# Performance work log

Hardware: AMD Instinct MI355X
Metric: run time of the kernel (lower is better)

The kernel has to match this reference:

```python
import jax, jax.numpy as jnp
import numpy as np

B, SQ, SE, H, NH = 2, 2048, 2048, 1024, 16
HD = H // NH  # 64

def setup_inputs() -> dict:
    key = jax.random.key(0)
    ks = jax.random.split(key, 8)
    s = 1.0 / np.sqrt(H)
    return {
        "hidden_states": jax.random.normal(ks[0], (B, SQ, H), jnp.float32),
        "encoder_hidden_states": jax.random.normal(ks[1], (B, SE, H), jnp.float32),
        "attention_mask": jnp.zeros((B, 1, 1, SQ + SE), jnp.float32),
        "Wq": jax.random.normal(ks[2], (H, H), jnp.float32) * s,
        "bq": jnp.zeros((H,), jnp.float32),
        "Wk": jax.random.normal(ks[3], (H, H), jnp.float32) * s,
        "bk": jnp.zeros((H,), jnp.float32),
        "Wv": jax.random.normal(ks[4], (H, H), jnp.float32) * s,
        "bv": jnp.zeros((H,), jnp.float32),
    }

def _split_heads(x):
    # [B, S, H] -> [B, NH, S, HD]
    b, s, _ = x.shape
    return x.reshape(b, s, NH, HD).transpose(0, 2, 1, 3)

def reference(hidden_states, encoder_hidden_states, attention_mask, Wq, bq, Wk, bk, Wv, bv):
    # Q from self tokens; K,V from concat(self, encoder) along sequence
    all_hs = jnp.concatenate([hidden_states, encoder_hidden_states], axis=1)  # [B, SQ+SE, H]
    q = _split_heads(hidden_states @ Wq + bq)   # [B, NH, SQ, HD]
    k = _split_heads(all_hs @ Wk + bk)          # [B, NH, SKV, HD]
    v = _split_heads(all_hs @ Wv + bv)          # [B, NH, SKV, HD]
    scores = jnp.einsum('bhqd,bhkd->bhqk', q, k) / jnp.sqrt(jnp.float32(HD))
    scores = scores + attention_mask            # additive mask, broadcast [B,1,1,SKV]
    probs = jax.nn.softmax(scores, axis=-1)     # dropout p=0 (eval)
    ctx = jnp.einsum('bhqk,bhkd->bhqd', probs, v)
    ctx = ctx.transpose(0, 2, 1, 3).reshape(hidden_states.shape[0], hidden_states.shape[1], H)
    return ctx
```

## Files before the change

### kernel.cpp

```cpp
#include <hip/hip_runtime.h>
#include <hip/hip_bf16.h>
#include <stdint.h>


typedef __attribute__((ext_vector_type(8))) short short8;
typedef __attribute__((ext_vector_type(4))) float f32x4;
typedef __attribute__((ext_vector_type(4))) unsigned short us4;

typedef __attribute__((ext_vector_type(8), may_alias)) short short8a;
typedef __attribute__((may_alias)) unsigned long long u64a;

#define MEMBAR() asm volatile("" ::: "memory")
#define DEV static __device__ __forceinline__

DEV unsigned short f2bf(float f) {
  unsigned int u = __builtin_bit_cast(unsigned int, f);
  u += 0x7fffu + ((u >> 16) & 1u);
  return (unsigned short)(u >> 16);
}

DEV float exp2_(float x) {
#if __has_builtin(__builtin_amdgcn_exp2f)
  return __builtin_amdgcn_exp2f(x);
#else
  float r; asm("v_exp_f32 %0, %1" : "=v"(r) : "v"(x)); return r;
#endif
}

DEV unsigned int cvtpk_bf16(float lo, float hi) {
  unsigned int r;
  asm("v_cvt_pk_bf16_f32 %0, %1, %2" : "=v"(r) : "v"(lo), "v"(hi));
  return r;
}

DEV void g2lds16(const void* g, void* l) {
  __builtin_amdgcn_global_load_lds((const __attribute__((address_space(1))) void*)g,
                                   (__attribute__((address_space(3))) void*)l, 16, 0, 0);
}

__global__ __launch_bounds__(256) void convert_allhs(const float* __restrict__ hid,
                                                     const float* __restrict__ enc,
                                                     unsigned short* __restrict__ ah) {
  int idx = blockIdx.x * 256 + threadIdx.x;
  const int perB = 4096 * 256;
  int b = idx / perB, r = idx - b * perB;
  int s = r >> 8, c4 = r & 255;
  const float* srcrow = (s < 2048) ? hid + (size_t)(b * 2048 + s) * 1024
                                   : enc + (size_t)(b * 2048 + (s - 2048)) * 1024;
  f32x4 v = *(const f32x4*)(srcrow + c4 * 4);
  us4 o;
  o[0] = f2bf(v[0]); o[1] = f2bf(v[1]); o[2] = f2bf(v[2]); o[3] = f2bf(v[3]);
  *(us4*)(ah + (size_t)idx * 4) = o;
}

__global__ __launch_bounds__(256) void premul_mask(const float* __restrict__ m,
                                                   float* __restrict__ o) {
  int i = blockIdx.x * 256 + threadIdx.x;
  o[i] = m[i] * 1.4426950408889634f;
}

__global__ __launch_bounds__(256) void transpose_w(const float* __restrict__ W,
                                                   unsigned short* __restrict__ Wt) {
  __shared__ unsigned short t[64][65];
  int k0 = blockIdx.y * 64, n0 = blockIdx.x * 64;
  int tid = threadIdx.x;
#pragma unroll
  for (int rep = 0; rep < 16; rep++) {
    int idx = rep * 256 + tid;
    int kk = idx >> 6, nn = idx & 63;
    t[kk][nn] = f2bf(W[(size_t)(k0 + kk) * 1024 + n0 + nn]);
  }
  __syncthreads();
#pragma unroll
  for (int rep = 0; rep < 16; rep++) {
    int idx = rep * 256 + tid;
    int nn = idx >> 6, kk = idx & 63;
    Wt[(size_t)(n0 + nn) * 1024 + k0 + kk] = t[kk][nn];
  }
}

template <int MODE>
__global__ __launch_bounds__(256) void gemm_nt(const unsigned short* __restrict__ R1, long r1bs,
                                               const unsigned short* __restrict__ R2, long r2bs,
                                               const float* __restrict__ bias,
                                               unsigned short* __restrict__ outp, long obs, int S,
                                               float oscale) {
  __shared__ unsigned short ldsA[128 * 32];
  __shared__ unsigned short ldsB[128 * 32];
  const int b = blockIdx.z;
  const unsigned short* A = R1 + (size_t)b * r1bs;
  const unsigned short* Bm = R2 + (size_t)b * r2bs;
  unsigned short* outb = outp + (size_t)b * obs;
  const int r0 = blockIdx.y * 128, c0 = blockIdx.x * 128;
  const int tid = threadIdx.x, w = tid >> 6, l = tid & 63;
  const int wr = w >> 1, wc = w & 1;
  const int lrow = l >> 2, lk = (l & 3) * 8;
  const int lc = l & 15, g = l >> 4;

  f32x4 acc[4][4];
#pragma unroll
  for (int i = 0; i < 4; i++)
#pragma unroll
    for (int j = 0; j < 4; j++) acc[i][j] = (f32x4){0.f, 0.f, 0.f, 0.f};

  for (int k0 = 0; k0 < 1024; k0 += 32) {
#pragma unroll
    for (int t = 0; t < 2; t++) {
      const int tt = w * 2 + t;
      g2lds16(A + (size_t)(r0 + tt * 16 + lrow) * 1024 + k0 + lk, (char*)ldsA + tt * 1024);
      g2lds16(Bm + (size_t)(c0 + tt * 16 + lrow) * 1024 + k0 + lk, (char*)ldsB + tt * 1024);
    }
    __syncthreads();
    short8 af[4], bf[4];
#pragma unroll
    for (int f = 0; f < 4; f++) {
      af[f] = *(const short8*)((const char*)ldsA + (wr * 64 + f * 16 + lc) * 64 + g * 16);
      bf[f] = *(const short8*)((const char*)ldsB + (wc * 64 + f * 16 + lc) * 64 + g * 16);
    }
#pragma unroll
    for (int fr = 0; fr < 4; fr++)
#pragma unroll
      for (int fc = 0; fc < 4; fc++)
        acc[fr][fc] = __builtin_amdgcn_mfma_f32_16x16x32_bf16(af[fr], bf[fc], acc[fr][fc], 0, 0, 0);
    __syncthreads();
  }

#pragma unroll
  for (int fr = 0; fr < 4; fr++) {
    int rb = r0 + wr * 64 + fr * 16 + g * 4;
    float bv[4];
    if (MODE == 0) {
#pragma unroll
      for (int i = 0; i < 4; i++) bv[i] = bias[rb + i];
    }
#pragma unroll
    for (int fc = 0; fc < 4; fc++) {
      int c = c0 + wc * 64 + fc * 16 + lc;
      float bc = (MODE == 0) ? 0.f : bias[c];
      us4 pk;
#pragma unroll
      for (int i = 0; i < 4; i++) {
        float v = (acc[fr][fc][i] + (MODE == 0 ? bv[i] : bc)) * oscale;
        pk[i] = f2bf(v);
      }
      size_t addr;
      if (MODE == 0) addr = ((size_t)(rb >> 6) * S + c) * 64 + (rb & 63);
      else           addr = (size_t)c * S + rb;
      *(us4*)(outb + addr) = pk;
    }
  }
}

__global__ __launch_bounds__(256) void attn_kernel(const unsigned short* __restrict__ Q,
                                                   const unsigned short* __restrict__ K,
                                                   const unsigned short* __restrict__ Vt,
                                                   const float* __restrict__ mask2,
                                                   float* __restrict__ out) {
  __shared__ __align__(16) char ldsKV[2][16384];
  __shared__ unsigned short plds[4096];

  int flat = blockIdx.x + 32 * (blockIdx.y + 16 * blockIdx.z);
  int xc = flat & 7, tt = flat >> 3;
  int f2 = xc * 64 + (tt & 63) + (tt >> 6) * 512;
  const int qt = f2 & 31, h = (f2 >> 5) & 15, b = f2 >> 9;

  const int tid = threadIdx.x, w = tid >> 6, l = tid & 63;
  const int lc = l & 15, g = l >> 4;

  const unsigned short* Qb = Q + ((size_t)(b * 16 + h) * 2048) * 64;
  const unsigned short* Kb = K + ((size_t)(b * 16 + h) * 4096) * 64;
  const unsigned short* Vb = Vt + ((size_t)(b * 16 + h) * 64) * 4096;
  const float* mk = mask2 + (size_t)b * 4096;
  const int sq0 = qt * 64 + w * 16;

  const int srow = l >> 3;
  const int schunk = (l & 7) ^ srow;

  short8 qf[2];
#pragma unroll
  for (int hh = 0; hh < 2; hh++)
    qf[hh] = *(const short8*)(Qb + (size_t)(sq0 + lc) * 64 + hh * 32 + g * 8);

  short8 ones;
#pragma unroll
  for (int i = 0; i < 8; i++) ones[i] = (short)0x3f80;

  f32x4 ctx[4];
#pragma unroll
  for (int df = 0; df < 4; df++) ctx[df] = (f32x4){0.f, 0.f, 0.f, 0.f};
  f32x4 lsacc = (f32x4){0.f, 0.f, 0.f, 0.f};

  char* pwave = (char*)plds + w * 2048;
  const int swz = (lc & 7) << 4;

  {
    char* kb = ldsKV[0];
    char* vb = ldsKV[0] + 8192;
#pragma unroll
    for (int c = 0; c < 2; c++) {
      int call = w * 2 + c;
      int r = call * 8 + srow;
      g2lds16(Kb + (size_t)r * 64 + schunk * 8, kb + call * 1024);
      g2lds16(Vb + (size_t)r * 4096 + schunk * 8, vb + call * 1024);
    }
  }
  __syncthreads();

  int bf = 0;
  for (int t = 0; t < 64; t++) {
    const int s0 = t * 64;
    f32x4 mvv[4];
#pragma unroll
    for (int f = 0; f < 4; f++)
      mvv[f] = *(const f32x4*)(mk + s0 + f * 16 + g * 4);

    if (t < 63) {
      char* kb = ldsKV[bf ^ 1];
      char* vb = ldsKV[bf ^ 1] + 8192;
#pragma unroll
      for (int c = 0; c < 2; c++) {
        int call = w * 2 + c;
        int r = call * 8 + srow;
        g2lds16(Kb + (size_t)(s0 + 64 + r) * 64 + schunk * 8, kb + call * 1024);
        g2lds16(Vb + (size_t)r * 4096 + (s0 + 64) + schunk * 8, vb + call * 1024);
      }
    }

    const char* kb = ldsKV[bf];
    const char* vb = ldsKV[bf] + 8192;

#pragma unroll
    for (int f = 0; f < 4; f++) {
      short8 k0 = *(const short8*)(kb + (f * 16 + lc) * 128 + ((g ^ (lc & 7)) << 4));
      short8 k1 = *(const short8*)(kb + (f * 16 + lc) * 128 + (((4 + g) ^ (lc & 7)) << 4));
      f32x4 z = __builtin_amdgcn_mfma_f32_16x16x32_bf16(k0, qf[0], mvv[f], 0, 0, 0);
      z = __builtin_amdgcn_mfma_f32_16x16x32_bf16(k1, qf[1], z, 0, 0, 0);
      unsigned int lo = cvtpk_bf16(exp2_(z[0]), exp2_(z[1]));
      unsigned int hi = cvtpk_bf16(exp2_(z[2]), exp2_(z[3]));
      int base = lc * 128 + f * 32 + g * 8;
      *(u64a*)(pwave + (base ^ swz)) = ((unsigned long long)hi << 32) | lo;
    }

    MEMBAR();

    short8 pfrag[2];
#pragma unroll
    for (int kk = 0; kk < 2; kk++)
      pfrag[kk] = (short8)*(const short8a*)(pwave + ((lc * 128 + kk * 64 + g * 16) ^ swz));
#pragma unroll
    for (int df = 0; df < 4; df++) {
      short8 v0 = *(const short8*)(vb + (df * 16 + lc) * 128 + ((g ^ (lc & 7)) << 4));
      short8 v1 = *(const short8*)(vb + (df * 16 + lc) * 128 + (((4 + g) ^ (lc & 7)) << 4));
      ctx[df] = __builtin_amdgcn_mfma_f32_16x16x32_bf16(v0, pfrag[0], ctx[df], 0, 0, 0);
      ctx[df] = __builtin_amdgcn_mfma_f32_16x16x32_bf16(v1, pfrag[1], ctx[df], 0, 0, 0);
    }
    lsacc = __builtin_amdgcn_mfma_f32_16x16x32_bf16(ones, pfrag[0], lsacc, 0, 0, 0);
    lsacc = __builtin_amdgcn_mfma_f32_16x16x32_bf16(ones, pfrag[1], lsacc, 0, 0, 0);

    __syncthreads();
    bf ^= 1;
  }

  float inv = 1.f / lsacc[0];
  size_t row = (size_t)(b * 2048 + sq0 + lc);
#pragma unroll
  for (int df = 0; df < 4; df++) {
    f32x4 o = ctx[df] * inv;
    *(f32x4*)(out + row * 1024 + h * 64 + df * 16 + g * 4) = o;
  }
}

extern "C" void kernel_launch(void* const* d_in, const int* in_sizes, int n_in,
                              void* d_out, int out_size, void* d_ws, size_t ws_size,
                              hipStream_t stream) {
  const float* hid = (const float*)d_in[0];
  const float* enc = (const float*)d_in[1];
  const float* mask = (const float*)d_in[2];
  const float* Wq = (const float*)d_in[3];
  const float* bq = (const float*)d_in[4];
  const float* Wk = (const float*)d_in[5];
  const float* bk = (const float*)d_in[6];
  const float* Wv = (const float*)d_in[7];
  const float* bv = (const float*)d_in[8];

  unsigned short* ws = (unsigned short*)d_ws;
  unsigned short* WTQ = ws;
  unsigned short* WTK = ws + 1048576;
  unsigned short* WTV = ws + 2097152;
  unsigned short* AH  = ws + 3145728;
  unsigned short* Qb  = ws + 11534336;
  unsigned short* Kb  = ws + 15728640;
  unsigned short* VT  = ws + 24117248;
  float* mask2 = (float*)(ws + 32505856);

  const float QSCALE = 0.18033688011112042f;

  convert_allhs<<<8192, 256, 0, stream>>>(hid, enc, AH);
  premul_mask<<<32, 256, 0, stream>>>(mask, mask2);
  transpose_w<<<dim3(16, 16), 256, 0, stream>>>(Wq, WTQ);
  transpose_w<<<dim3(16, 16), 256, 0, stream>>>(Wk, WTK);
  transpose_w<<<dim3(16, 16), 256, 0, stream>>>(Wv, WTV);

  gemm_nt<0><<<dim3(16, 8, 2), 256, 0, stream>>>(WTQ, 0, AH, 4194304, bq, Qb, 2097152, 2048, QSCALE);
  gemm_nt<0><<<dim3(32, 8, 2), 256, 0, stream>>>(WTK, 0, AH, 4194304, bk, Kb, 4194304, 4096, 1.0f);
  gemm_nt<1><<<dim3(8, 32, 2), 256, 0, stream>>>(AH, 4194304, WTV, 0, bv, VT, 4194304, 4096, 1.0f);

  attn_kernel<<<dim3(32, 16, 2), 256, 0, stream>>>(Qb, Kb, VT, mask2, (float*)d_out);
}
```

Baseline: 215.6 us.

## Merge QKV GEMMs and weight transposes into single launches; load V directly

The three weight-transpose kernels become one launch over a z dimension, and the three projection GEMMs become a single 1280-block kernel that picks Q/K/V work from a remapped block id with runtime mode selection. This cuts launch count and tail effects between the GEMMs. In the attention kernel, V fragments are now read straight from global memory into registers each iteration instead of being staged through double-buffered LDS, which halves LDS use. The direct V loads may expose global latency inside the loop, and the runtime mode branch adds a little epilogue overhead.

```diff
diff --git a/kernel.cpp b/kernel.cpp
--- a/kernel.cpp
+++ b/kernel.cpp
@@ -59,9 +59,14 @@
   o[i] = m[i] * 1.4426950408889634f;
 }
 
-__global__ __launch_bounds__(256) void transpose_w(const float* __restrict__ W,
-                                                   unsigned short* __restrict__ Wt) {
+__global__ __launch_bounds__(256) void transpose_w3(const float* __restrict__ Wq,
+                                                    const float* __restrict__ Wk,
+                                                    const float* __restrict__ Wv,
+                                                    unsigned short* __restrict__ WtBase) {
   __shared__ unsigned short t[64][65];
+  const int z = blockIdx.z;
+  const float* W = (z == 0) ? Wq : (z == 1) ? Wk : Wv;
+  unsigned short* Wt = WtBase + (size_t)z * 1048576;
   int k0 = blockIdx.y * 64, n0 = blockIdx.x * 64;
   int tid = threadIdx.x;
 #pragma unroll
@@ -79,19 +84,48 @@
   }
 }
 
-template <int MODE>
-__global__ __launch_bounds__(256) void gemm_nt(const unsigned short* __restrict__ R1, long r1bs,
-                                               const unsigned short* __restrict__ R2, long r2bs,
-                                               const float* __restrict__ bias,
-                                               unsigned short* __restrict__ outp, long obs, int S,
-                                               float oscale) {
+__global__ __launch_bounds__(256) void gemm_all(const unsigned short* __restrict__ WTQ,
+                                                const unsigned short* __restrict__ WTK,
+                                                const unsigned short* __restrict__ WTV,
+                                                const unsigned short* __restrict__ AH,
+                                                const float* __restrict__ bq,
+                                                const float* __restrict__ bk,
+                                                const float* __restrict__ bv,
+                                                unsigned short* __restrict__ Qout,
+                                                unsigned short* __restrict__ Kout,
+                                                unsigned short* __restrict__ Vout,
+                                                float qscale) {
   __shared__ unsigned short ldsA[128 * 32];
   __shared__ unsigned short ldsB[128 * 32];
-  const int b = blockIdx.z;
-  const unsigned short* A = R1 + (size_t)b * r1bs;
-  const unsigned short* Bm = R2 + (size_t)b * r2bs;
-  unsigned short* outb = outp + (size_t)b * obs;
-  const int r0 = blockIdx.y * 128, c0 = blockIdx.x * 128;
+
+  int id = blockIdx.x;
+  int f2 = (id & 7) * 160 + (id >> 3);
+
+  const unsigned short *A, *Bm;
+  const float* bias;
+  unsigned short* outb;
+  int S, mode, r0, c0;
+  float osc = 1.0f;
+  if (f2 < 256) {
+    int t = f2;
+    int b = t >> 7; t &= 127;
+    c0 = (t & 15) * 128; r0 = (t >> 4) * 128;
+    A = WTQ; Bm = AH + (size_t)b * 4194304; bias = bq;
+    outb = Qout + (size_t)b * 2097152; S = 2048; mode = 0; osc = qscale;
+  } else if (f2 < 768) {
+    int t = f2 - 256;
+    int b = t >> 8; t &= 255;
+    c0 = (t & 31) * 128; r0 = (t >> 5) * 128;
+    A = WTK; Bm = AH + (size_t)b * 4194304; bias = bk;
+    outb = Kout + (size_t)b * 4194304; S = 4096; mode = 0;
+  } else {
+    int t = f2 - 768;
+    int b = t >> 8; t &= 255;
+    c0 = (t & 7) * 128; r0 = (t >> 3) * 128;
+    A = AH + (size_t)b * 4194304; Bm = WTV; bias = bv;
+    outb = Vout + (size_t)b * 4194304; S = 4096; mode = 1;
+  }
+
   const int tid = threadIdx.x, w = tid >> 6, l = tid & 63;
   const int wr = w >> 1, wc = w & 1;
   const int lrow = l >> 2, lk = (l & 3) * 8;
@@ -128,23 +162,23 @@
 #pragma unroll
   for (int fr = 0; fr < 4; fr++) {
     int rb = r0 + wr * 64 + fr * 16 + g * 4;
-    float bv[4];
-    if (MODE == 0) {
-#pragma unroll
-      for (int i = 0; i < 4; i++) bv[i] = bias[rb + i];
+    float bv4[4];
+    if (mode == 0) {
+#pragma unroll
+      for (int i = 0; i < 4; i++) bv4[i] = bias[rb + i];
     }
 #pragma unroll
     for (int fc = 0; fc < 4; fc++) {
       int c = c0 + wc * 64 + fc * 16 + lc;
-      float bc = (MODE == 0) ? 0.f : bias[c];
+      float bc = (mode == 0) ? 0.f : bias[c];
       us4 pk;
 #pragma unroll
       for (int i = 0; i < 4; i++) {
-        float v = (acc[fr][fc][i] + (MODE == 0 ? bv[i] : bc)) * oscale;
+        float v = (acc[fr][fc][i] + (mode == 0 ? bv4[i] : bc)) * osc;
         pk[i] = f2bf(v);
       }
       size_t addr;
-      if (MODE == 0) addr = ((size_t)(rb >> 6) * S + c) * 64 + (rb & 63);
+      if (mode == 0) addr = ((size_t)(rb >> 6) * S + c) * 64 + (rb & 63);
       else           addr = (size_t)c * S + rb;
       *(us4*)(outb + addr) = pk;
     }
@@ -156,7 +190,7 @@
                                                    const unsigned short* __restrict__ Vt,
                                                    const float* __restrict__ mask2,
                                                    float* __restrict__ out) {
-  __shared__ __align__(16) char ldsKV[2][16384];
+  __shared__ __align__(16) char ldsK[2][8192];
   __shared__ unsigned short plds[4096];
 
   int flat = blockIdx.x + 32 * (blockIdx.y + 16 * blockIdx.z);
@@ -194,14 +228,11 @@
   const int swz = (lc & 7) << 4;
 
   {
-    char* kb = ldsKV[0];
-    char* vb = ldsKV[0] + 8192;
 #pragma unroll
     for (int c = 0; c < 2; c++) {
       int call = w * 2 + c;
       int r = call * 8 + srow;
-      g2lds16(Kb + (size_t)r * 64 + schunk * 8, kb + call * 1024);
-      g2lds16(Vb + (size_t)r * 4096 + schunk * 8, vb + call * 1024);
+      g2lds16(Kb + (size_t)r * 64 + schunk * 8, ldsK[0] + call * 1024);
     }
   }
   __syncthreads();
@@ -209,25 +240,29 @@
   int bf = 0;
   for (int t = 0; t < 64; t++) {
     const int s0 = t * 64;
-    f32x4 mvv[4];
-#pragma unroll
-    for (int f = 0; f < 4; f++)
-      mvv[f] = *(const f32x4*)(mk + s0 + f * 16 + g * 4);
 
     if (t < 63) {
-      char* kb = ldsKV[bf ^ 1];
-      char* vb = ldsKV[bf ^ 1] + 8192;
 #pragma unroll
       for (int c = 0; c < 2; c++) {
         int call = w * 2 + c;
         int r = call * 8 + srow;
-        g2lds16(Kb + (size_t)(s0 + 64 + r) * 64 + schunk * 8, kb + call * 1024);
-        g2lds16(Vb + (size_t)r * 4096 + (s0 + 64) + schunk * 8, vb + call * 1024);
+        g2lds16(Kb + (size_t)(s0 + 64 + r) * 64 + schunk * 8, ldsK[bf ^ 1] + call * 1024);
       }
     }
 
-    const char* kb = ldsKV[bf];
-    const char* vb = ldsKV[bf] + 8192;
+    short8 vf[4][2];
+#pragma unroll
+    for (int df = 0; df < 4; df++)
+#pragma unroll
+      for (int kk = 0; kk < 2; kk++)
+        vf[df][kk] = *(const short8*)(Vb + (size_t)(df * 16 + lc) * 4096 + s0 + kk * 32 + g * 8);
+
+    f32x4 mvv[4];
+#pragma unroll
+    for (int f = 0; f < 4; f++)
+      mvv[f] = *(const f32x4*)(mk + s0 + f * 16 + g * 4);
+
+    const char* kb = ldsK[bf];
 
 #pragma unroll
     for (int f = 0; f < 4; f++) {
@@ -249,10 +284,8 @@
       pfrag[kk] = (short8)*(const short8a*)(pwave + ((lc * 128 + kk * 64 + g * 16) ^ swz));
 #pragma unroll
     for (int df = 0; df < 4; df++) {
-      short8 v0 = *(const short8*)(vb + (df * 16 + lc) * 128 + ((g ^ (lc & 7)) << 4));
-      short8 v1 = *(const short8*)(vb + (df * 16 + lc) * 128 + (((4 + g) ^ (lc & 7)) << 4));
-      ctx[df] = __builtin_amdgcn_mfma_f32_16x16x32_bf16(v0, pfrag[0], ctx[df], 0, 0, 0);
-      ctx[df] = __builtin_amdgcn_mfma_f32_16x16x32_bf16(v1, pfrag[1], ctx[df], 0, 0, 0);
+      ctx[df] = __builtin_amdgcn_mfma_f32_16x16x32_bf16(vf[df][0], pfrag[0], ctx[df], 0, 0, 0);
+      ctx[df] = __builtin_amdgcn_mfma_f32_16x16x32_bf16(vf[df][1], pfrag[1], ctx[df], 0, 0, 0);
     }
     lsacc = __builtin_amdgcn_mfma_f32_16x16x32_bf16(ones, pfrag[0], lsacc, 0, 0, 0);
     lsacc = __builtin_amdgcn_mfma_f32_16x16x32_bf16(ones, pfrag[1], lsacc, 0, 0, 0);
@@ -297,13 +330,9 @@
 
   convert_allhs<<<8192, 256, 0, stream>>>(hid, enc, AH);
   premul_mask<<<32, 256, 0, stream>>>(mask, mask2);
-  transpose_w<<<dim3(16, 16), 256, 0, stream>>>(Wq, WTQ);
-  transpose_w<<<dim3(16, 16), 256, 0, stream>>>(Wk, WTK);
-  transpose_w<<<dim3(16, 16), 256, 0, stream>>>(Wv, WTV);
-
-  gemm_nt<0><<<dim3(16, 8, 2), 256, 0, stream>>>(WTQ, 0, AH, 4194304, bq, Qb, 2097152, 2048, QSCALE);
-  gemm_nt<0><<<dim3(32, 8, 2), 256, 0, stream>>>(WTK, 0, AH, 4194304, bk, Kb, 4194304, 4096, 1.0f);
-  gemm_nt<1><<<dim3(8, 32, 2), 256, 0, stream>>>(AH, 4194304, WTV, 0, bv, VT, 4194304, 4096, 1.0f);
+  transpose_w3<<<dim3(16, 16, 3), 256, 0, stream>>>(Wq, Wk, Wv, WTQ);
+
+  gemm_all<<<1280, 256, 0, stream>>>(WTQ, WTK, WTV, AH, bq, bk, bv, Qb, Kb, VT, QSCALE);
 
   attn_kernel<<<dim3(32, 16, 2), 256, 0, stream>>>(Qb, Kb, VT, mask2, (float*)d_out);
 }
```

Result: slower. 370.9 us (+72.1%).
